# Kernel optimization log

Measured on AMD Instinct MI355X. Metric: run time of the kernel, lower is better.

The kernel has to match this reference:

```python
import jax, jax.numpy as jnp
import numpy as np

B, S, DE = 64, 512, 384
D, M, H, NH = 1024, 16, 4, 8
DA, DO, T_MAX = 512, 512, 16


def setup_inputs() -> dict:
    key = jax.random.key(0)
    ks = jax.random.split(key, 24)
    n = lambda k, sh, s=0.02: (jax.random.normal(k, sh) * s).astype(jnp.float32)
    z = lambda sh: jnp.zeros(sh, jnp.float32)
    return {
        'embeddings': jax.random.normal(ks[0], (B, S, DE), jnp.float32),
        'Wp': n(ks[1], (D, DE)), 'bp': z(D), 'ln_g': jnp.ones(D, jnp.float32), 'ln_b': z(D),
        'decay_a': z(DA), 'decay_o': z(DO),
        'Wq': n(ks[2], (D, DA)), 'bq': z(D),
        'Wqkv': n(ks[3], (3 * D, D)), 'bqkv': z(3 * D),
        'Wo': n(ks[4], (D, D)), 'bo': z(D),
        'Ws1': n(ks[5], (2 * D, 2 * D)), 'bs1': z(2 * D),
        'Ws2': n(ks[6], (D, 2 * D)), 'bs2': z(D),
        'Wn1': n(ks[7], (D, H, M), 0.1), 'bn1': z((D, H)),
        'Wn2': n(ks[8], (D, H, H), 0.1), 'bn2': z((D, H)),
        'Wn3': n(ks[9], (D, H), 0.1), 'bn3': z(D),
        'Wh1': n(ks[10], (DO, DO)), 'bh1': z(DO),
        'Wh2': n(ks[11], (1, DO)), 'bh2': z(1),
        'z_init': n(ks[12], (1, D)), 'hist_init': z((1, D, M)),
        'idx_i_a': jax.random.randint(ks[13], (DA,), 0, D),
        'idx_j_a': jax.random.randint(ks[14], (DA,), 0, D),
        'idx_i_o': jax.random.randint(ks[15], (DO,), 0, D),
        'idx_j_o': jax.random.randint(ks[16], (DO,), 0, D),
    }


def _gelu(x):
    return jax.nn.gelu(x, approximate=False)  # torch nn.GELU default = exact erf


def _forward(embeddings, Wp, bp, ln_g, ln_b, decay_a, decay_o, Wq, bq, Wqkv, bqkv,
             Wo, bo, Ws1, bs1, Ws2, bs2, Wn1, bn1, Wn2, bn2, Wn3, bn3,
             Wh1, bh1, Wh2, bh2, z_init, hist_init,
             idx_i_a, idx_j_a, idx_i_o, idx_j_o):
    Bb = embeddings.shape[0]
    # input_proj: Linear + LayerNorm + GELU
    h = embeddings @ Wp.T + bp
    mu = h.mean(-1, keepdims=True)
    var = ((h - mu) ** 2).mean(-1, keepdims=True)
    ctx = _gelu((h - mu) * jax.lax.rsqrt(var + 1e-5) * ln_g + ln_b)  # [B,S,D]

    Wq3, Wk3, Wv3 = jnp.split(Wqkv, 3, axis=0)
    bq3, bk3, bv3 = jnp.split(bqkv, 3, axis=0)
    dh = D // NH
    scale = 1.0 / np.sqrt(dh).astype(np.float32)
    # K/V of ctx are loop-invariant (MHA recomputes them each tick; math identical)
    k = (ctx @ Wk3.T + bk3).reshape(Bb, -1, NH, dh)
    v = (ctx @ Wv3.T + bv3).reshape(Bb, -1, NH, dh)

    soft_a = jax.nn.softplus(decay_a)
    soft_o = jax.nn.softplus(decay_o)
    z0 = jnp.broadcast_to(z_init, (Bb, D))
    hist0 = jnp.broadcast_to(hist_init, (Bb, D, M))
    zbuf0 = jnp.zeros((Bb, T_MAX + 1, D), ctx.dtype).at[:, 0].set(z0)
    ts_all = jnp.arange(T_MAX + 1, dtype=jnp.float32)

    def sync(zbuf, t, soft, ii, jj):
        # age of history slot s at tick t is (t - s); mask future/unwritten slots
        age = t.astype(jnp.float32) - ts_all                      # [T+1]
        w = jnp.where(age[:, None] >= 0, jnp.exp(-soft[None, :] * age[:, None]), 0.0)  # [T+1,Ds]
        zi = zbuf[:, :, ii]
        zj = zbuf[:, :, jj]                                        # [B,T+1,Ds]
        num = jnp.einsum('bts,ts->bs', zi * zj, w)
        den = jnp.sqrt(jnp.sum(w * w, axis=0) + 1e-8)
        return num / den

    def step(carry, t):
        z, hist, zbuf = carry
        s_act = sync(zbuf, t, soft_a, idx_i_a, idx_j_a)            # [B,DA]
        s_out = sync(zbuf, t, soft_o, idx_i_o, idx_j_o)            # [B,DO]
        q = s_act @ Wq.T + bq                                      # query_proj -> [B,D]
        qh = (q @ Wq3.T + bq3).reshape(Bb, NH, dh)
        att = jax.nn.softmax(jnp.einsum('bhd,bshd->bhs', qh, k) * scale, axis=-1)
        attn_out = jnp.einsum('bhs,bshd->bhd', att, v).reshape(Bb, D) @ Wo.T + bo
        combined = jnp.concatenate([z, attn_out], axis=-1)          # [B,2D]
        pre = _gelu(combined @ Ws1.T + bs1) @ Ws2.T + bs2           # synapse (dropout=eval)
        hist = jnp.concatenate([hist[:, :, 1:], pre[:, :, None]], axis=-1)
        # grouped-conv NLM: per-neuron MLP over its M-history
        x = _gelu(jnp.einsum('bdm,dhm->bdh', hist, Wn1) + bn1)
        x = _gelu(jnp.einsum('bdh,dgh->bdg', x, Wn2) + bn2)
        z_new = jnp.einsum('bdh,dh->bd', x, Wn3) + bn3              # [B,D]
        zbuf = jax.lax.dynamic_update_slice(zbuf, z_new[:, None, :], (0, t + 1, 0))
        logits = _gelu(s_out @ Wh1.T + bh1) @ Wh2.T + bh2           # head -> [B,1]
        return (z_new, hist, zbuf), logits

    _, logits_seq = jax.lax.scan(step, (z0, hist0, zbuf0), jnp.arange(T_MAX))
    return jnp.transpose(logits_seq, (1, 0, 2))  # all_logits [B,T_max,1]


def reference(embeddings, Wp, bp, ln_g, ln_b, decay_a, decay_o, Wq, bq, Wqkv, bqkv,
              Wo, bo, Ws1, bs1, Ws2, bs2, Wn1, bn1, Wn2, bn2, Wn3, bn3,
              Wh1, bh1, Wh2, bh2, z_init, hist_init,
              idx_i_a, idx_j_a, idx_i_o, idx_j_o):
    return _forward(embeddings, Wp, bp, ln_g, ln_b, decay_a, decay_o, Wq, bq, Wqkv, bqkv,
                    Wo, bo, Ws1, bs1, Ws2, bs2, Wn1, bn1, Wn2, bn2, Wn3, bn3,
                    Wh1, bh1, Wh2, bh2, z_init, hist_init,
                    idx_i_a, idx_j_a, idx_i_o, idx_j_o)
```

## Files before the change

kernel.cpp:

```cpp
#include <hip/hip_runtime.h>
#include <hip/hip_bf16.h>

constexpr int CB = 64;
constexpr int CS = 512;
constexpr int CDE = 384;
constexpr int CD = 1024;
constexpr int CM = 16;
constexpr int CH = 4;
constexpr int CNH = 8;
constexpr int CDH = 128;
constexpr int CDA = 512;
constexpr int CDO = 512;
constexpr int CT = 16;
constexpr int CTP1 = 17;

typedef __attribute__((ext_vector_type(8))) short bfrag;
typedef __attribute__((ext_vector_type(4))) float ffrag;

__device__ __forceinline__ float gelu_exact(float x) {
    return 0.5f * x * (1.0f + erff(x * 0.70710678118654752440f));
}
__device__ __forceinline__ float softplusf(float x) {
    return fmaxf(x, 0.0f) + log1pf(expf(-fabsf(x)));
}
__device__ __forceinline__ float us2f(unsigned short u) {
    union { unsigned int i; float f; } c; c.i = ((unsigned int)u) << 16; return c.f;
}
__device__ __forceinline__ unsigned short f2us(float x) {
    __hip_bfloat16 b = __float2bfloat16(x);
    union { __hip_bfloat16 b; unsigned short u; } c; c.b = b; return c.u;
}

template <typename T>
__device__ __forceinline__ float4 ld4(const T* p);
template <>
__device__ __forceinline__ float4 ld4<float>(const float* p) { return *(const float4*)p; }
template <>
__device__ __forceinline__ float4 ld4<unsigned short>(const unsigned short* p) {
    ushort4 u = *(const ushort4*)p;
    return make_float4(us2f(u.x), us2f(u.y), us2f(u.z), us2f(u.w));
}
__device__ __forceinline__ void st4(float* p, float4 v) { *(float4*)p = v; }
__device__ __forceinline__ void st4(unsigned short* p, float4 v) {
    ushort4 u = make_ushort4(f2us(v.x), f2us(v.y), f2us(v.z), f2us(v.w));
    *(ushort4*)p = u;
}

__device__ __forceinline__ bfrag ld8bf(const unsigned short* p) {
    return *(const bfrag*)p;
}
__device__ __forceinline__ bfrag ld8bf(const float* p) {
    float4 a = *(const float4*)p;
    float4 b = *(const float4*)(p + 4);
    bfrag v;
    v[0] = (short)f2us(a.x); v[1] = (short)f2us(a.y);
    v[2] = (short)f2us(a.z); v[3] = (short)f2us(a.w);
    v[4] = (short)f2us(b.x); v[5] = (short)f2us(b.y);
    v[6] = (short)f2us(b.z); v[7] = (short)f2us(b.w);
    return v;
}

__global__ __launch_bounds__(256) void convert_bf16_kernel(
    const float* __restrict__ src, unsigned short* __restrict__ dst, int n4) {
    int i = blockIdx.x * 256 + threadIdx.x;
    if (i < n4) {
        float4 v = *(const float4*)(src + (size_t)i * 4);
        st4(dst + (size_t)i * 4, v);
    }
}

__global__ __launch_bounds__(256) void transpose_wq_kernel(
    const float* __restrict__ Wq, unsigned short* __restrict__ WqT) {
    int i = blockIdx.x * 256 + threadIdx.x;
    if (i < CDA * CD) {
        int a = i / CD, d = i - a * CD;
        WqT[i] = f2us(Wq[(size_t)d * CDA + a]);
    }
}

__global__ __launch_bounds__(256) void transpose_wo_kernel(
    const float* __restrict__ Wo, unsigned short* __restrict__ WoT) {
    int i = blockIdx.x * 256 + threadIdx.x;
    if (i < CD * CD) {
        int d = i >> 10, k = i & 1023;
        WoT[i] = f2us(Wo[(size_t)k * CD + d]);
    }
}

__global__ __launch_bounds__(256) void pack_ws1_kernel(
    const float* __restrict__ Ws1, unsigned short* __restrict__ ws1a,
    unsigned short* __restrict__ ws1b) {
    int i = blockIdx.x * 256 + threadIdx.x;
    if (i < 2 * CD * CD) {
        int j = i >> 10, k = i & 1023;
        ws1a[i] = f2us(Ws1[(size_t)j * (2 * CD) + k]);
        ws1b[i] = f2us(Ws1[(size_t)j * (2 * CD) + CD + k]);
    }
}

__global__ __launch_bounds__(256) void beff_kernel(
    const float* __restrict__ Wqkv, const float* __restrict__ bq,
    const float* __restrict__ bqkv, float* __restrict__ beff) {
    int i = blockIdx.x * 256 + threadIdx.x;
    if (i < CD) {
        const float* w = Wqkv + (size_t)i * CD;
        float s = bqkv[i];
        for (int d = 0; d < CD; d += 4) {
            float4 wv = *(const float4*)(w + d);
            s += wv.x * bq[d] + wv.y * bq[d + 1] + wv.z * bq[d + 2] + wv.w * bq[d + 3];
        }
        beff[i] = s;
    }
}

__global__ __launch_bounds__(256) void beff1_kernel(
    const float* __restrict__ Ws1, const float* __restrict__ bo,
    const float* __restrict__ bs1, float* __restrict__ beff1) {
    int j = blockIdx.x * 256 + threadIdx.x;
    if (j < 2 * CD) {
        const float* w = Ws1 + (size_t)j * (2 * CD) + CD;
        float s = bs1[j];
        for (int k = 0; k < CD; k += 4) {
            float4 wv = *(const float4*)(w + k);
            s += wv.x * bo[k] + wv.y * bo[k + 1] + wv.z * bo[k + 2] + wv.w * bo[k + 3];
        }
        beff1[j] = s;
    }
}

__global__ __launch_bounds__(256) void transpose_v_kernel(
    const unsigned short* __restrict__ vbuf, unsigned short* __restrict__ vT) {
    __shared__ unsigned short tile[64][65];
    int bid = blockIdx.x;
    int bh = bid >> 4;
    int tl = bid & 15;
    int s0 = (tl >> 1) * 64, d0 = (tl & 1) * 64;
    int b = bh >> 3, h = bh & 7;
    int sl = threadIdx.x >> 6, dl = threadIdx.x & 63;
#pragma unroll
    for (int it = 0; it < 16; it++) {
        int s = s0 + it * 4 + sl;
        tile[it * 4 + sl][dl] = vbuf[((size_t)(b * CS + s)) * CD + h * CDH + d0 + dl];
    }
    __syncthreads();
    int s2 = threadIdx.x & 63, dr = threadIdx.x >> 6;
#pragma unroll
    for (int it = 0; it < 16; it++) {
        int d = it * 4 + dr;
        vT[((size_t)(bh * CDH + d0 + d)) * CS + s0 + s2] = tile[s2][d];
    }
}

template <typename TA, typename TW>
__global__ __launch_bounds__(256) void gemm_mfma(
    const TA* __restrict__ A, const TW* __restrict__ W,
    const float* __restrict__ bias, unsigned short* __restrict__ C,
    int N, int K) {
    __shared__ __align__(16) char smem[32768];
    char* As = smem;
    char* Bs = smem + 16384;
    const int tid = threadIdx.x;
    const int row0 = blockIdx.x << 7;
    const int col0 = blockIdx.y << 7;
    const int lane = tid & 63;
    const int wid = tid >> 6;
    const int wr = wid >> 1, wc = wid & 1;
    const int srow_l = tid >> 3;
    const int schunk = tid & 7;

    ffrag acc[4][4];
#pragma unroll
    for (int m = 0; m < 4; m++)
#pragma unroll
        for (int n = 0; n < 4; n++) acc[m][n] = (ffrag)0.0f;

    for (int k0 = 0; k0 < K; k0 += 64) {
        bfrag va[4], vb[4];
#pragma unroll
        for (int i = 0; i < 4; i++) {
            int r = i * 32 + srow_l;
            va[i] = ld8bf(A + (size_t)(row0 + r) * K + k0 + schunk * 8);
            vb[i] = ld8bf(W + (size_t)(col0 + r) * K + k0 + schunk * 8);
        }
#pragma unroll
        for (int i = 0; i < 4; i++) {
            int r = i * 32 + srow_l;
            int pc = schunk ^ (r & 7);
            *(bfrag*)(As + r * 128 + pc * 16) = va[i];
            *(bfrag*)(Bs + r * 128 + pc * 16) = vb[i];
        }
        __syncthreads();
#pragma unroll
        for (int s = 0; s < 2; s++) {
            bfrag af[4], bf[4];
#pragma unroll
            for (int m = 0; m < 4; m++) {
                int r = wr * 64 + m * 16 + (lane & 15);
                int chunk = (s * 4 + (lane >> 4)) ^ (r & 7);
                af[m] = *(const bfrag*)(As + r * 128 + chunk * 16);
            }
#pragma unroll
            for (int n = 0; n < 4; n++) {
                int r = wc * 64 + n * 16 + (lane & 15);
                int chunk = (s * 4 + (lane >> 4)) ^ (r & 7);
                bf[n] = *(const bfrag*)(Bs + r * 128 + chunk * 16);
            }
#pragma unroll
            for (int m = 0; m < 4; m++)
#pragma unroll
                for (int n = 0; n < 4; n++)
                    acc[m][n] = __builtin_amdgcn_mfma_f32_16x16x32_bf16(
                        af[m], bf[n], acc[m][n], 0, 0, 0);
        }
        __syncthreads();
    }

#pragma unroll
    for (int n = 0; n < 4; n++) {
        int col = col0 + wc * 64 + n * 16 + (lane & 15);
        float bv = bias[col];
#pragma unroll
        for (int m = 0; m < 4; m++) {
            int rbase = row0 + wr * 64 + m * 16 + ((lane >> 4) << 2);
#pragma unroll
            for (int j = 0; j < 4; j++) {
                C[(size_t)(rbase + j) * N + col] = f2us(acc[m][n][j] + bv);
            }
        }
    }
}

__global__ __launch_bounds__(256) void gemm64k(
    const unsigned short* __restrict__ A, const unsigned short* __restrict__ W,
    float* __restrict__ P, int N, int K, int kc) {
    __shared__ __align__(16) char smem[16384];
    char* As = smem;
    char* Bs = smem + 8192;
    const int tid = threadIdx.x;
    const int col0 = blockIdx.x << 6;
    const int kbeg = blockIdx.y * kc;
    const int lane = tid & 63;
    const int wv = tid >> 6;
    const int srow = tid >> 3;
    const int schunk = tid & 7;

    ffrag acc[4];
#pragma unroll
    for (int n = 0; n < 4; n++) acc[n] = (ffrag)0.0f;

    for (int k0 = kbeg; k0 < kbeg + kc; k0 += 64) {
        bfrag va[2], vb[2];
#pragma unroll
        for (int i = 0; i < 2; i++) {
            int r = i * 32 + srow;
            va[i] = *(const bfrag*)(A + (size_t)r * K + k0 + schunk * 8);
            vb[i] = *(const bfrag*)(W + (size_t)(col0 + r) * K + k0 + schunk * 8);
        }
#pragma unroll
        for (int i = 0; i < 2; i++) {
            int r = i * 32 + srow;
            int pc = schunk ^ (r & 7);
            *(bfrag*)(As + r * 128 + pc * 16) = va[i];
            *(bfrag*)(Bs + r * 128 + pc * 16) = vb[i];
        }
        __syncthreads();
#pragma unroll
        for (int s = 0; s < 2; s++) {
            int r = wv * 16 + (lane & 15);
            int ch = (s * 4 + (lane >> 4)) ^ (r & 7);
            bfrag af = *(const bfrag*)(As + r * 128 + ch * 16);
#pragma unroll
            for (int n = 0; n < 4; n++) {
                int r2 = n * 16 + (lane & 15);
                int ch2 = (s * 4 + (lane >> 4)) ^ (r2 & 7);
                bfrag bf = *(const bfrag*)(Bs + r2 * 128 + ch2 * 16);
                acc[n] = __builtin_amdgcn_mfma_f32_16x16x32_bf16(af, bf, acc[n], 0, 0, 0);
            }
        }
        __syncthreads();
    }

    float* Pz = P + (size_t)blockIdx.y * 64 * N;
#pragma unroll
    for (int n = 0; n < 4; n++) {
        int col = col0 + n * 16 + (lane & 15);
        int rbase = wv * 16 + ((lane >> 4) << 2);
#pragma unroll
        for (int j = 0; j < 4; j++) {
            Pz[(size_t)(rbase + j) * N + col] = acc[n][j];
        }
    }
}

__global__ __launch_bounds__(256) void ln_gelu_kernel(
    unsigned short* __restrict__ hc, const float* __restrict__ g,
    const float* __restrict__ bb) {
    __shared__ float sred[4];
    const int tid = threadIdx.x;
    size_t base = (size_t)blockIdx.x * CD;
    float4 x = ld4(hc + base + tid * 4);
    float s = x.x + x.y + x.z + x.w;
#pragma unroll
    for (int off = 32; off; off >>= 1) s += __shfl_down(s, off, 64);
    if ((tid & 63) == 0) sred[tid >> 6] = s;
    __syncthreads();
    float mu = (sred[0] + sred[1] + sred[2] + sred[3]) * (1.0f / 1024.0f);
    float d0 = x.x - mu, d1 = x.y - mu, d2 = x.z - mu, d3 = x.w - mu;
    float sq = d0 * d0 + d1 * d1 + d2 * d2 + d3 * d3;
    __syncthreads();
#pragma unroll
    for (int off = 32; off; off >>= 1) sq += __shfl_down(sq, off, 64);
    if ((tid & 63) == 0) sred[tid >> 6] = sq;
    __syncthreads();
    float var = (sred[0] + sred[1] + sred[2] + sred[3]) * (1.0f / 1024.0f);
    float rs = 1.0f / sqrtf(var + 1e-5f);
    float4 gv = ((const float4*)g)[tid];
    float4 bv = ((const float4*)bb)[tid];
    float4 o;
    o.x = gelu_exact(d0 * rs * gv.x + bv.x);
    o.y = gelu_exact(d1 * rs * gv.y + bv.y);
    o.z = gelu_exact(d2 * rs * gv.z + bv.z);
    o.w = gelu_exact(d3 * rs * gv.w + bv.w);
    st4(hc + base + tid * 4, o);
}

__global__ __launch_bounds__(256) void init_kernel(
    const float* __restrict__ z_init, const float* __restrict__ hist_init,
    float* __restrict__ zbufT, float* __restrict__ hist) {
    int i = blockIdx.x * 256 + threadIdx.x;
    if (i < CB * CD * CTP1) {
        int rem = i % (CD * CTP1);
        int d = rem / CTP1;
        int ts = rem - d * CTP1;
        zbufT[i] = (ts == 0) ? z_init[d] : 0.0f;
    }
    if (i < CB * CD * CM) {
        hist[i] = hist_init[i % (CD * CM)];
    }
}

__global__ __launch_bounds__(256) void sync_kernel(
    const float* __restrict__ zbufT,
    const float* __restrict__ decay_a, const float* __restrict__ decay_o,
    const int* __restrict__ iia, const int* __restrict__ jja,
    const int* __restrict__ iio, const int* __restrict__ jjo,
    unsigned short* __restrict__ s_act, float* __restrict__ s_out,
    unsigned short* __restrict__ zb16, int t) {
    int b = blockIdx.x >> 2;
    int sg = ((blockIdx.x & 3) << 8) + threadIdx.x;
    const float* zbT = zbufT + (size_t)b * CD * CTP1;
    zb16[b * CD + sg] = f2us(zbT[(size_t)sg * CTP1 + t]);
    float soft;
    int ii, jj;
    if (sg < CDA) {
        soft = softplusf(decay_a[sg]);
        ii = iia[sg]; jj = jja[sg];
    } else {
        int s2 = sg - CDA;
        soft = softplusf(decay_o[s2]);
        ii = iio[s2]; jj = jjo[s2];
    }
    const float* zi = zbT + (size_t)ii * CTP1;
    const float* zj = zbT + (size_t)jj * CTP1;
    float num = 0.0f, den = 0.0f;
    for (int ts = 0; ts <= t; ts++) {
        float w = expf(-soft * (float)(t - ts));
        num += zi[ts] * zj[ts] * w;
        den += w * w;
    }
    float val = num / sqrtf(den + 1e-8f);
    if (sg < CDA) s_act[b * CDA + sg] = f2us(val);
    else s_out[b * CDO + (sg - CDA)] = val;
}

__global__ __launch_bounds__(512) void attn512_kernel(
    const float* __restrict__ Pq, const float* __restrict__ beff,
    const unsigned short* __restrict__ kb, const unsigned short* __restrict__ vT,
    unsigned short* __restrict__ attn_out) {
    __shared__ __align__(16) char smraw[43648];
    char* buf0 = smraw;
    char* buf1 = smraw + 18432;
    float* att  = (float*)(smraw + 36864);
    float* qv   = (float*)(smraw + 38912);
    float* pacc = (float*)(smraw + 39424);
    float* ppv  = (float*)(smraw + 41472);
    float* red  = (float*)(smraw + 43520);
    const int tid = threadIdx.x;
    const int lane = tid & 63;
    const int wv = tid >> 6;
    const int pair = blockIdx.x;
    const int b = pair >> 3, h = pair & 7;
    const float scale = 0.08838834764831845f;

    if (tid < CDH) {
        int col = h * CDH + tid;
        float q = beff[col];
#pragma unroll
        for (int z = 0; z < 8; z++) q += Pq[((size_t)(z * 64 + b)) * CD + col];
        qv[tid] = q;
    }

    const unsigned short* kbase = kb + (size_t)(b * CS) * CD + h * CDH;
    const int sR0 = tid >> 4, c16 = tid & 15;
    {
        bfrag a = *(const bfrag*)(kbase + (size_t)sR0 * CD + c16 * 8);
        bfrag bb = *(const bfrag*)(kbase + (size_t)(sR0 + 32) * CD + c16 * 8);
        *(bfrag*)(buf0 + sR0 * 272 + c16 * 16) = a;
        *(bfrag*)(buf0 + (sR0 + 32) * 272 + c16 * 16) = bb;
    }
    __syncthreads();
    const int sC = tid & 63, g = wv;
    for (int c = 0; c < 8; c++) {
        char* cur = (c & 1) ? buf1 : buf0;
        char* nxt = (c & 1) ? buf0 : buf1;
        bfrag pa, pb;
        if (c < 7) {
            pa = *(const bfrag*)(kbase + (size_t)((c + 1) * 64 + sR0) * CD + c16 * 8);
            pb = *(const bfrag*)(kbase + (size_t)((c + 1) * 64 + sR0 + 32) * CD + c16 * 8);
        }
        {
            bfrag k0 = *(const bfrag*)(cur + sC * 272 + g * 32);
            bfrag k1 = *(const bfrag*)(cur + sC * 272 + g * 32 + 16);
            float s = 0.0f;
#pragma unroll
            for (int e = 0; e < 8; e++) {
                s += us2f((unsigned short)k0[e]) * qv[g * 16 + e];
                s += us2f((unsigned short)k1[e]) * qv[g * 16 + 8 + e];
            }
            pacc[g * 64 + sC] = s;
        }
        __syncthreads();
        if (c < 7) {
            *(bfrag*)(nxt + sR0 * 272 + c16 * 16) = pa;
            *(bfrag*)(nxt + (sR0 + 32) * 272 + c16 * 16) = pb;
        }
        if (tid < 64) {
            float s = 0.0f;
#pragma unroll
            for (int gg = 0; gg < 8; gg++) s += pacc[gg * 64 + tid];
            att[c * 64 + tid] = s * scale;
        }
        __syncthreads();
    }

    const unsigned short* vbase = vT + (size_t)((b * CNH + h) * CDH) * CS;
    const int dR0 = tid >> 3, c8 = tid & 7;
    bfrag v0a = *(const bfrag*)(vbase + (size_t)dR0 * CS + c8 * 8);
    bfrag v0b = *(const bfrag*)(vbase + (size_t)(dR0 + 64) * CS + c8 * 8);

    {
        float v = att[tid];
        float m = v;
#pragma unroll
        for (int o = 32; o; o >>= 1) m = fmaxf(m, __shfl_down(m, o, 64));
        if (lane == 0) red[wv] = m;
        __syncthreads();
        float mx = red[0];
#pragma unroll
        for (int r = 1; r < 8; r++) mx = fmaxf(mx, red[r]);
        float e = expf(v - mx);
        float s = e;
#pragma unroll
        for (int o = 32; o; o >>= 1) s += __shfl_down(s, o, 64);
        __syncthreads();
        if (lane == 0) red[8 + wv] = s;
        __syncthreads();
        float tot = 0.0f;
#pragma unroll
        for (int r = 0; r < 8; r++) tot += red[8 + r];
        att[tid] = e / tot;
    }
    *(bfrag*)(buf0 + dR0 * 144 + c8 * 16) = v0a;
    *(bfrag*)(buf0 + (dR0 + 64) * 144 + c8 * 16) = v0b;
    __syncthreads();

    const int dC = tid & 127, q = tid >> 7;
    float pv = 0.0f;
    for (int c = 0; c < 8; c++) {
        char* cur = (c & 1) ? buf1 : buf0;
        char* nxt = (c & 1) ? buf0 : buf1;
        bfrag pa, pb;
        if (c < 7) {
            pa = *(const bfrag*)(vbase + (size_t)dR0 * CS + (c + 1) * 64 + c8 * 8);
            pb = *(const bfrag*)(vbase + (size_t)(dR0 + 64) * CS + (c + 1) * 64 + c8 * 8);
        }
        {
            bfrag w0 = *(const bfrag*)(cur + dC * 144 + q * 32);
            bfrag w1 = *(const bfrag*)(cur + dC * 144 + q * 32 + 16);
            const float* ap = att + c * 64 + q * 16;
#pragma unroll
            for (int e = 0; e < 8; e++) {
                pv += us2f((unsigned short)w0[e]) * ap[e];
                pv += us2f((unsigned short)w1[e]) * ap[8 + e];
            }
        }
        __syncthreads();
        if (c < 7) {
            *(bfrag*)(nxt + dR0 * 144 + c8 * 16) = pa;
            *(bfrag*)(nxt + (dR0 + 64) * 144 + c8 * 16) = pb;
        }
        __syncthreads();
    }
    ppv[q * 128 + dC] = pv;
    __syncthreads();
    if (tid < CDH) {
        float o = ppv[tid] + ppv[128 + tid] + ppv[256 + tid] + ppv[384 + tid];
        attn_out[(size_t)b * CD + h * CDH + tid] = f2us(o);
    }
}

__global__ __launch_bounds__(256) void pre1r_kernel(
    const float* __restrict__ P2, const float* __restrict__ P3,
    const float* __restrict__ beff1, unsigned short* __restrict__ pre1) {
    int i = blockIdx.x * 256 + threadIdx.x;
    int j = i & 2047;
    float v = beff1[j];
#pragma unroll
    for (int z = 0; z < 8; z++)
        v += P2[(size_t)z * 131072 + i] + P3[(size_t)z * 131072 + i];
    pre1[i] = f2us(gelu_exact(v));
}

__global__ __launch_bounds__(256) void ws2r_neuron_kernel(
    const float* __restrict__ Pw, const float* __restrict__ bs2,
    float* __restrict__ hist,
    const float* __restrict__ Wn1, const float* __restrict__ bn1,
    const float* __restrict__ Wn2, const float* __restrict__ bn2,
    const float* __restrict__ Wn3, const float* __restrict__ bn3,
    float* __restrict__ zbufT, int t) {
    int idx = blockIdx.x * 256 + threadIdx.x;
    int d = idx & 1023;
    float prev = bs2[d];
#pragma unroll
    for (int z = 0; z < 8; z++) prev += Pw[(size_t)z * 65536 + idx];
    float hv[CM];
    float* hp = hist + (size_t)idx * CM;
#pragma unroll
    for (int m = 0; m < CM - 1; m++) hv[m] = hp[m + 1];
    hv[CM - 1] = prev;
#pragma unroll
    for (int m = 0; m < CM; m++) hp[m] = hv[m];
    float x1[CH];
#pragma unroll
    for (int hh = 0; hh < CH; hh++) {
        const float* w = Wn1 + ((size_t)d * CH + hh) * CM;
        float s = bn1[d * CH + hh];
#pragma unroll
        for (int m = 0; m < CM; m++) s += hv[m] * w[m];
        x1[hh] = gelu_exact(s);
    }
    float x2[CH];
#pragma unroll
    for (int g = 0; g < CH; g++) {
        float s = bn2[d * CH + g];
#pragma unroll
        for (int hh = 0; hh < CH; hh++) s += x1[hh] * Wn2[((size_t)d * CH + g) * CH + hh];
        x2[g] = gelu_exact(s);
    }
    float z = bn3[d];
#pragma unroll
    for (int hh = 0; hh < CH; hh++) z += x2[hh] * Wn3[d * CH + hh];
    zbufT[(size_t)idx * CTP1 + (t + 1)] = z;
}

__global__ __launch_bounds__(256) void logits_kernel(
    const float* __restrict__ s_out, const unsigned short* __restrict__ Wh1b,
    const float* __restrict__ bh1, const float* __restrict__ Wh2,
    const float* __restrict__ bh2, float* __restrict__ out, int t) {
    __shared__ float so[CDO];
    __shared__ float hh[CDO];
    __shared__ float red[4];
    const int b = blockIdx.x, tid = threadIdx.x;
    ((float2*)so)[tid] = ((const float2*)(s_out + (size_t)b * CDO))[tid];
    __syncthreads();
#pragma unroll
    for (int p = 0; p < 2; p++) {
        int j = tid + p * 256;
        const unsigned short* w = Wh1b + (size_t)j * CDO;
        float s = bh1[j];
#pragma unroll 4
        for (int k2 = 0; k2 < CDO; k2 += 4) {
            float4 wv = ld4(w + k2);
            s += wv.x * so[k2] + wv.y * so[k2 + 1] + wv.z * so[k2 + 2] + wv.w * so[k2 + 3];
        }
        hh[j] = gelu_exact(s);
    }
    __syncthreads();
    float part = hh[tid] * Wh2[tid] + hh[tid + 256] * Wh2[tid + 256];
#pragma unroll
    for (int off = 32; off; off >>= 1) part += __shfl_down(part, off, 64);
    if ((tid & 63) == 0) red[tid >> 6] = part;
    __syncthreads();
    if (tid == 0) out[b * CT + t] = red[0] + red[1] + red[2] + red[3] + bh2[0];
}

__global__ void sentinel_kernel(float* out, float v) {
    int i = blockIdx.x * 256 + threadIdx.x;
    if (i < CB * CT) out[i] = v;
}

extern "C" void kernel_launch(void* const* d_in, const int* in_sizes, int n_in,
                              void* d_out, int out_size, void* d_ws, size_t ws_size,
                              hipStream_t stream) {
    const float* emb = (const float*)d_in[0];
    const float* Wp = (const float*)d_in[1];
    const float* bp = (const float*)d_in[2];
    const float* ln_g = (const float*)d_in[3];
    const float* ln_b = (const float*)d_in[4];
    const float* decay_a = (const float*)d_in[5];
    const float* decay_o = (const float*)d_in[6];
    const float* Wq = (const float*)d_in[7];
    const float* bq = (const float*)d_in[8];
    const float* Wqkv = (const float*)d_in[9];
    const float* bqkv = (const float*)d_in[10];
    const float* Wo = (const float*)d_in[11];
    const float* bo = (const float*)d_in[12];
    const float* Ws1 = (const float*)d_in[13];
    const float* bs1 = (const float*)d_in[14];
    const float* Ws2 = (const float*)d_in[15];
    const float* bs2 = (const float*)d_in[16];
    const float* Wn1 = (const float*)d_in[17];
    const float* bn1 = (const float*)d_in[18];
    const float* Wn2 = (const float*)d_in[19];
    const float* bn2 = (const float*)d_in[20];
    const float* Wn3 = (const float*)d_in[21];
    const float* bn3 = (const float*)d_in[22];
    const float* Wh1 = (const float*)d_in[23];
    const float* bh1 = (const float*)d_in[24];
    const float* Wh2 = (const float*)d_in[25];
    const float* bh2 = (const float*)d_in[26];
    const float* z_init = (const float*)d_in[27];
    const float* hist_init = (const float*)d_in[28];
    const int* iia = (const int*)d_in[29];
    const int* jja = (const int*)d_in[30];
    const int* iio = (const int*)d_in[31];
    const int* jjo = (const int*)d_in[32];
    float* out = (float*)d_out;

    char* wsb = (char*)d_ws;
    size_t off = 0;
    auto alloc = [&](size_t bytes) {
        void* p = wsb + off;
        off += (bytes + 255) & ~(size_t)255;
        return p;
    };
    unsigned short* ctx  = (unsigned short*)alloc((size_t)CB * CS * CD * 2);
    unsigned short* kbuf = (unsigned short*)alloc((size_t)CB * CS * CD * 2);
    unsigned short* vbuf = (unsigned short*)alloc((size_t)CB * CS * CD * 2);
    float* zbufT = (float*)alloc((size_t)CB * CD * CTP1 * 4);
    float* hist = (float*)alloc((size_t)CB * CD * CM * 4);
    unsigned short* s_act = (unsigned short*)alloc((size_t)CB * CDA * 2);
    float* s_out = (float*)alloc((size_t)CB * CDO * 4);
    unsigned short* zb16 = (unsigned short*)alloc((size_t)CB * CD * 2);
    unsigned short* attn_out = (unsigned short*)alloc((size_t)CB * CD * 2);
    unsigned short* pre1 = (unsigned short*)alloc((size_t)CB * 2 * CD * 2);
    float* Pq = (float*)alloc((size_t)8 * 64 * CD * 4);
    float* P2 = (float*)alloc((size_t)8 * 64 * 2 * CD * 4);
    float* P3 = (float*)alloc((size_t)8 * 64 * 2 * CD * 4);
    unsigned short* wqkv_b = (unsigned short*)alloc((size_t)3 * CD * CD * 2);
    unsigned short* ws2_b = (unsigned short*)alloc((size_t)CD * 2 * CD * 2);
    unsigned short* wh1_b = (unsigned short*)alloc((size_t)CDO * CDO * 2);
    unsigned short* wqT_b = (unsigned short*)alloc((size_t)CDA * CD * 2);
    unsigned short* weff_b = (unsigned short*)alloc((size_t)CD * CDA * 2);
    unsigned short* ws1a_b = (unsigned short*)alloc((size_t)2 * CD * CD * 2);
    unsigned short* ws1b_b = (unsigned short*)alloc((size_t)2 * CD * CD * 2);
    unsigned short* woT_b = (unsigned short*)alloc((size_t)CD * CD * 2);
    unsigned short* weff2_b = (unsigned short*)alloc((size_t)2 * CD * CD * 2);
    float* beff = (float*)alloc((size_t)CD * 4);
    float* beff1 = (float*)alloc((size_t)2 * CD * 4);
    float* zbias = (float*)alloc((size_t)2 * CD * 4);
    unsigned short* vT = ctx;

    if (off > ws_size) {
        sentinel_kernel<<<dim3(4), dim3(256), 0, stream>>>(out, -(float)(ws_size >> 20));
        return;
    }

    auto conv = [&](const float* s, unsigned short* d, size_t n) {
        int n4 = (int)(n / 4);
        convert_bf16_kernel<<<dim3((n4 + 255) / 256), 256, 0, stream>>>(s, d, n4);
    };
    conv(Wqkv, wqkv_b, (size_t)3 * CD * CD);
    conv(Ws2, ws2_b, (size_t)CD * 2 * CD);
    conv(Wh1, wh1_b, (size_t)CDO * CDO);
    transpose_wq_kernel<<<dim3((CDA * CD + 255) / 256), 256, 0, stream>>>(Wq, wqT_b);
    transpose_wo_kernel<<<dim3((CD * CD + 255) / 256), 256, 0, stream>>>(Wo, woT_b);
    pack_ws1_kernel<<<dim3((2 * CD * CD + 255) / 256), 256, 0, stream>>>(Ws1, ws1a_b, ws1b_b);
    hipMemsetAsync(zbias, 0, (size_t)2 * CD * 4, stream);
    beff_kernel<<<dim3(4), 256, 0, stream>>>(Wqkv, bq, bqkv, beff);
    beff1_kernel<<<dim3(8), 256, 0, stream>>>(Ws1, bo, bs1, beff1);
    gemm_mfma<unsigned short, unsigned short><<<dim3(CD / 128, CDA / 128), 256, 0, stream>>>(
        wqkv_b, wqT_b, zbias, weff_b, CDA, CD);
    gemm_mfma<unsigned short, unsigned short><<<dim3(2 * CD / 128, CD / 128), 256, 0, stream>>>(
        ws1b_b, woT_b, zbias, weff2_b, CD, CD);

    gemm_mfma<float, float><<<dim3(CB * CS / 128, CD / 128), 256, 0, stream>>>(
        emb, Wp, bp, ctx, CD, CDE);
    ln_gelu_kernel<<<dim3(CB * CS), 256, 0, stream>>>(ctx, ln_g, ln_b);
    gemm_mfma<unsigned short, unsigned short><<<dim3(CB * CS / 128, CD / 128), 256, 0, stream>>>(
        ctx, wqkv_b + (size_t)CD * CD, bqkv + CD, kbuf, CD, CD);
    gemm_mfma<unsigned short, unsigned short><<<dim3(CB * CS / 128, CD / 128), 256, 0, stream>>>(
        ctx, wqkv_b + (size_t)2 * CD * CD, bqkv + 2 * CD, vbuf, CD, CD);
    transpose_v_kernel<<<dim3(CB * CNH * 16), 256, 0, stream>>>(vbuf, vT);
    init_kernel<<<dim3(4352), 256, 0, stream>>>(z_init, hist_init, zbufT, hist);

    for (int t = 0; t < CT; t++) {
        sync_kernel<<<dim3(256), 256, 0, stream>>>(
            zbufT, decay_a, decay_o, iia, jja, iio, jjo, s_act, s_out, zb16, t);
        logits_kernel<<<dim3(CB), 256, 0, stream>>>(s_out, wh1_b, bh1, Wh2, bh2, out, t);
        gemm64k<<<dim3(16, 8), 256, 0, stream>>>(s_act, weff_b, Pq, CD, CDA, CDA / 8);
        gemm64k<<<dim3(32, 8), 256, 0, stream>>>(zb16, ws1a_b, P2, 2 * CD, CD, CD / 8);
        attn512_kernel<<<dim3(CB * CNH), 512, 0, stream>>>(Pq, beff, kbuf, vT, attn_out);
        gemm64k<<<dim3(32, 8), 256, 0, stream>>>(attn_out, weff2_b, P3, 2 * CD, CD, CD / 8);
        pre1r_kernel<<<dim3(512), 256, 0, stream>>>(P2, P3, beff1, pre1);
        gemm64k<<<dim3(16, 8), 256, 0, stream>>>(pre1, ws2_b, Pq, CD, 2 * CD, 2 * CD / 8);
        ws2r_neuron_kernel<<<dim3(256), 256, 0, stream>>>(
            Pq, bs2, hist, Wn1, bn1, Wn2, bn2, Wn3, bn3, zbufT, t);
    }
}
```

Before: 1.680 ms.

## Fuse q-projection into attention and merge Ws1 GEMMs via concatenated K

Moves the per-step q projection (s_act times weff) into the attention kernel, which removes one split-K GEMM launch and its partial-sum buffer. The z and attention-output activations are written into one concatenated [B,2D] buffer, and the two Ws1-side weights are packed into one [2D,2D] matrix, so a single GEMM with K=2048 replaces two K=1024 GEMMs and the P3 reduction. The setup GEMM also gains a grouped workgroup swizzle and a column offset and stride for writing into the concatenated weight. This cuts per-step launches and partial-sum traffic, but each attention block now recomputes its q slice with scalar bf16 dot products.

```diff
diff --git a/kernel.cpp b/kernel.cpp
--- a/kernel.cpp
+++ b/kernel.cpp
@@ -88,12 +88,12 @@
 }
 
 __global__ __launch_bounds__(256) void pack_ws1_kernel(
-    const float* __restrict__ Ws1, unsigned short* __restrict__ ws1a,
+    const float* __restrict__ Ws1, unsigned short* __restrict__ wcat,
     unsigned short* __restrict__ ws1b) {
     int i = blockIdx.x * 256 + threadIdx.x;
     if (i < 2 * CD * CD) {
         int j = i >> 10, k = i & 1023;
-        ws1a[i] = f2us(Ws1[(size_t)j * (2 * CD) + k]);
+        wcat[(size_t)j * (2 * CD) + k] = f2us(Ws1[(size_t)j * (2 * CD) + k]);
         ws1b[i] = f2us(Ws1[(size_t)j * (2 * CD) + CD + k]);
     }
 }
@@ -155,13 +155,16 @@
 __global__ __launch_bounds__(256) void gemm_mfma(
     const TA* __restrict__ A, const TW* __restrict__ W,
     const float* __restrict__ bias, unsigned short* __restrict__ C,
-    int N, int K) {
+    int K, int coff, int CW) {
     __shared__ __align__(16) char smem[32768];
     char* As = smem;
     char* Bs = smem + 16384;
     const int tid = threadIdx.x;
-    const int row0 = blockIdx.x << 7;
-    const int col0 = blockIdx.y << 7;
+    int flat = blockIdx.y * gridDim.x + blockIdx.x;
+    int nwg = gridDim.x * gridDim.y;
+    int swz = ((nwg & 7) == 0) ? ((flat & 7) * (nwg >> 3) + (flat >> 3)) : flat;
+    const int row0 = (swz % gridDim.x) << 7;
+    const int col0 = (swz / gridDim.x) << 7;
     const int lane = tid & 63;
     const int wid = tid >> 6;
     const int wr = wid >> 1, wc = wid & 1;
@@ -224,7 +227,7 @@
             int rbase = row0 + wr * 64 + m * 16 + ((lane >> 4) << 2);
 #pragma unroll
             for (int j = 0; j < 4; j++) {
-                C[(size_t)(rbase + j) * N + col] = f2us(acc[m][n][j] + bv);
+                C[(size_t)(rbase + j) * CW + coff + col] = f2us(acc[m][n][j] + bv);
             }
         }
     }
@@ -345,11 +348,11 @@
     const int* __restrict__ iia, const int* __restrict__ jja,
     const int* __restrict__ iio, const int* __restrict__ jjo,
     unsigned short* __restrict__ s_act, float* __restrict__ s_out,
-    unsigned short* __restrict__ zb16, int t) {
+    unsigned short* __restrict__ acat, int t) {
     int b = blockIdx.x >> 2;
     int sg = ((blockIdx.x & 3) << 8) + threadIdx.x;
     const float* zbT = zbufT + (size_t)b * CD * CTP1;
-    zb16[b * CD + sg] = f2us(zbT[(size_t)sg * CTP1 + t]);
+    acat[(size_t)b * (2 * CD) + sg] = f2us(zbT[(size_t)sg * CTP1 + t]);
     float soft;
     int ii, jj;
     if (sg < CDA) {
@@ -374,9 +377,10 @@
 }
 
 __global__ __launch_bounds__(512) void attn512_kernel(
-    const float* __restrict__ Pq, const float* __restrict__ beff,
+    const unsigned short* __restrict__ s_act, const unsigned short* __restrict__ weff,
+    const float* __restrict__ beff,
     const unsigned short* __restrict__ kb, const unsigned short* __restrict__ vT,
-    unsigned short* __restrict__ attn_out) {
+    unsigned short* __restrict__ acat) {
     __shared__ __align__(16) char smraw[43648];
     char* buf0 = smraw;
     char* buf1 = smraw + 18432;
@@ -392,23 +396,33 @@
     const int b = pair >> 3, h = pair & 7;
     const float scale = 0.08838834764831845f;
 
-    if (tid < CDH) {
-        int col = h * CDH + tid;
-        float q = beff[col];
-#pragma unroll
-        for (int z = 0; z < 8; z++) q += Pq[((size_t)(z * 64 + b)) * CD + col];
-        qv[tid] = q;
-    }
-
     const unsigned short* kbase = kb + (size_t)(b * CS) * CD + h * CDH;
     const int sR0 = tid >> 4, c16 = tid & 15;
     {
         bfrag a = *(const bfrag*)(kbase + (size_t)sR0 * CD + c16 * 8);
         bfrag bb = *(const bfrag*)(kbase + (size_t)(sR0 + 32) * CD + c16 * 8);
+        const int col = tid & 127, ks = tid >> 7;
+        const unsigned short* wr = weff + (size_t)(h * CDH + col) * CDA + ks * 128;
+        const unsigned short* sa = s_act + (size_t)b * CDA + ks * 128;
+        float s = 0.0f;
+#pragma unroll
+        for (int e8 = 0; e8 < 128; e8 += 8) {
+            bfrag wvv = *(const bfrag*)(wr + e8);
+            bfrag av = *(const bfrag*)(sa + e8);
+#pragma unroll
+            for (int e = 0; e < 8; e++)
+                s += us2f((unsigned short)wvv[e]) * us2f((unsigned short)av[e]);
+        }
+        pacc[ks * 128 + col] = s;
         *(bfrag*)(buf0 + sR0 * 272 + c16 * 16) = a;
         *(bfrag*)(buf0 + (sR0 + 32) * 272 + c16 * 16) = bb;
     }
     __syncthreads();
+    if (tid < CDH)
+        qv[tid] = beff[h * CDH + tid] + pacc[tid] + pacc[128 + tid] +
+                  pacc[256 + tid] + pacc[384 + tid];
+    __syncthreads();
+
     const int sC = tid & 63, g = wv;
     for (int c = 0; c < 8; c++) {
         char* cur = (c & 1) ? buf1 : buf0;
@@ -505,19 +519,18 @@
     __syncthreads();
     if (tid < CDH) {
         float o = ppv[tid] + ppv[128 + tid] + ppv[256 + tid] + ppv[384 + tid];
-        attn_out[(size_t)b * CD + h * CDH + tid] = f2us(o);
+        acat[(size_t)b * (2 * CD) + CD + h * CDH + tid] = f2us(o);
     }
 }
 
 __global__ __launch_bounds__(256) void pre1r_kernel(
-    const float* __restrict__ P2, const float* __restrict__ P3,
-    const float* __restrict__ beff1, unsigned short* __restrict__ pre1) {
+    const float* __restrict__ P2, const float* __restrict__ beff1,
+    unsigned short* __restrict__ pre1) {
     int i = blockIdx.x * 256 + threadIdx.x;
     int j = i & 2047;
     float v = beff1[j];
 #pragma unroll
-    for (int z = 0; z < 8; z++)
-        v += P2[(size_t)z * 131072 + i] + P3[(size_t)z * 131072 + i];
+    for (int z = 0; z < 8; z++) v += P2[(size_t)z * 131072 + i];
     pre1[i] = f2us(gelu_exact(v));
 }
 
@@ -651,21 +664,18 @@
     float* hist = (float*)alloc((size_t)CB * CD * CM * 4);
     unsigned short* s_act = (unsigned short*)alloc((size_t)CB * CDA * 2);
     float* s_out = (float*)alloc((size_t)CB * CDO * 4);
-    unsigned short* zb16 = (unsigned short*)alloc((size_t)CB * CD * 2);
-    unsigned short* attn_out = (unsigned short*)alloc((size_t)CB * CD * 2);
+    unsigned short* acat = (unsigned short*)alloc((size_t)CB * 2 * CD * 2);
     unsigned short* pre1 = (unsigned short*)alloc((size_t)CB * 2 * CD * 2);
-    float* Pq = (float*)alloc((size_t)8 * 64 * CD * 4);
+    float* Pw = (float*)alloc((size_t)8 * 64 * CD * 4);
     float* P2 = (float*)alloc((size_t)8 * 64 * 2 * CD * 4);
-    float* P3 = (float*)alloc((size_t)8 * 64 * 2 * CD * 4);
     unsigned short* wqkv_b = (unsigned short*)alloc((size_t)3 * CD * CD * 2);
     unsigned short* ws2_b = (unsigned short*)alloc((size_t)CD * 2 * CD * 2);
     unsigned short* wh1_b = (unsigned short*)alloc((size_t)CDO * CDO * 2);
     unsigned short* wqT_b = (unsigned short*)alloc((size_t)CDA * CD * 2);
     unsigned short* weff_b = (unsigned short*)alloc((size_t)CD * CDA * 2);
-    unsigned short* ws1a_b = (unsigned short*)alloc((size_t)2 * CD * CD * 2);
     unsigned short* ws1b_b = (unsigned short*)alloc((size_t)2 * CD * CD * 2);
     unsigned short* woT_b = (unsigned short*)alloc((size_t)CD * CD * 2);
-    unsigned short* weff2_b = (unsigned short*)alloc((size_t)2 * CD * CD * 2);
+    unsigned short* wcat = (unsigned short*)alloc((size_t)2 * CD * 2 * CD * 2);
     float* beff = (float*)alloc((size_t)CD * 4);
     float* beff1 = (float*)alloc((size_t)2 * CD * 4);
     float* zbias = (float*)alloc((size_t)2 * CD * 4);
@@ -685,36 +695,35 @@
     conv(Wh1, wh1_b, (size_t)CDO * CDO);
     transpose_wq_kernel<<<dim3((CDA * CD + 255) / 256), 256, 0, stream>>>(Wq, wqT_b);
     transpose_wo_kernel<<<dim3((CD * CD + 255) / 256), 256, 0, stream>>>(Wo, woT_b);
-    pack_ws1_kernel<<<dim3((2 * CD * CD + 255) / 256), 256, 0, stream>>>(Ws1, ws1a_b, ws1b_b);
+    pack_ws1_kernel<<<dim3((2 * CD * CD + 255) / 256), 256, 0, stream>>>(Ws1, wcat, ws1b_b);
     hipMemsetAsync(zbias, 0, (size_t)2 * CD * 4, stream);
     beff_kernel<<<dim3(4), 256, 0, stream>>>(Wqkv, bq, bqkv, beff);
     beff1_kernel<<<dim3(8), 256, 0, stream>>>(Ws1, bo, bs1, beff1);
     gemm_mfma<unsigned short, unsigned short><<<dim3(CD / 128, CDA / 128), 256, 0, stream>>>(
-        wqkv_b, wqT_b, zbias, weff_b, CDA, CD);
+        wqkv_b, wqT_b, zbias, weff_b, CD, 0, CDA);
     gemm_mfma<unsigned short, unsigned short><<<dim3(2 * CD / 128, CD / 128), 256, 0, stream>>>(
-        ws1b_b, woT_b, zbias, weff2_b, CD, CD);
+        ws1b_b, woT_b, zbias, wcat, CD, CD, 2 * CD);
 
     gemm_mfma<float, float><<<dim3(CB * CS / 128, CD / 128), 256, 0, stream>>>(
-        emb, Wp, bp, ctx, CD, CDE);
+        emb, Wp, bp, ctx, CDE, 0, CD);
     ln_gelu_kernel<<<dim3(CB * CS), 256, 0, stream>>>(ctx, ln_g, ln_b);
     gemm_mfma<unsigned short, unsigned short><<<dim3(CB * CS / 128, CD / 128), 256, 0, stream>>>(
-        ctx, wqkv_b + (size_t)CD * CD, bqkv + CD, kbuf, CD, CD);
+        ctx, wqkv_b + (size_t)CD * CD, bqkv + CD, kbuf, CD, 0, CD);
     gemm_mfma<unsigned short, unsigned short><<<dim3(CB * CS / 128, CD / 128), 256, 0, stream>>>(
-        ctx, wqkv_b + (size_t)2 * CD * CD, bqkv + 2 * CD, vbuf, CD, CD);
+        ctx, wqkv_b + (size_t)2 * CD * CD, bqkv + 2 * CD, vbuf, CD, 0, CD);
     transpose_v_kernel<<<dim3(CB * CNH * 16), 256, 0, stream>>>(vbuf, vT);
     init_kernel<<<dim3(4352), 256, 0, stream>>>(z_init, hist_init, zbufT, hist);
 
     for (int t = 0; t < CT; t++) {
         sync_kernel<<<dim3(256), 256, 0, stream>>>(
-            zbufT, decay_a, decay_o, iia, jja, iio, jjo, s_act, s_out, zb16, t);
+            zbufT, decay_a, decay_o, iia, jja, iio, jjo, s_act, s_out, acat, t);
         logits_kernel<<<dim3(CB), 256, 0, stream>>>(s_out, wh1_b, bh1, Wh2, bh2, out, t);
-        gemm64k<<<dim3(16, 8), 256, 0, stream>>>(s_act, weff_b, Pq, CD, CDA, CDA / 8);
-        gemm64k<<<dim3(32, 8), 256, 0, stream>>>(zb16, ws1a_b, P2, 2 * CD, CD, CD / 8);
-        attn512_kernel<<<dim3(CB * CNH), 512, 0, stream>>>(Pq, beff, kbuf, vT, attn_out);
-        gemm64k<<<dim3(32, 8), 256, 0, stream>>>(attn_out, weff2_b, P3, 2 * CD, CD, CD / 8);
-        pre1r_kernel<<<dim3(512), 256, 0, stream>>>(P2, P3, beff1, pre1);
-        gemm64k<<<dim3(16, 8), 256, 0, stream>>>(pre1, ws2_b, Pq, CD, 2 * CD, 2 * CD / 8);
+        attn512_kernel<<<dim3(CB * CNH), 512, 0, stream>>>(
+            s_act, weff_b, beff, kbuf, vT, acat);
+        gemm64k<<<dim3(32, 8), 256, 0, stream>>>(acat, wcat, P2, 2 * CD, 2 * CD, 2 * CD / 8);
+        pre1r_kernel<<<dim3(512), 256, 0, stream>>>(P2, beff1, pre1);
+        gemm64k<<<dim3(16, 8), 256, 0, stream>>>(pre1, ws2_b, Pw, CD, 2 * CD, 2 * CD / 8);
         ws2r_neuron_kernel<<<dim3(256), 256, 0, stream>>>(
-            Pq, bs2, hist, Wn1, bn1, Wn2, bn2, Wn3, bn3, zbufT, t);
-    }
-}
+            Pw, bs2, hist, Wn1, bn1, Wn2, bn2, Wn3, bn3, zbufT, t);
+    }
+}
```

Result: slower. 1.721 ms (+2.4%).
